# Performance work log

Measured on AMD Instinct MI355X. Metric: run time of the kernel, lower is better.

## Reference

```python
import jax, jax.numpy as jnp
import numpy as np

MAX_LENGTH = 11
SOS_TOKEN = 0
H = 256      # hidden_dim
V = 32000    # output_dim (vocab)
B = 256      # batch
S = 64       # encoder seq len


def setup_inputs() -> dict:
    key = jax.random.key(0)
    ks = jax.random.split(key, 16)
    sc = 0.05
    return {
        "encoder_outputs": jax.random.normal(ks[0], (B, S, H), jnp.float32),
        "encoder_hidden": jax.random.normal(ks[1], (1, B, H), jnp.float32),
        "target_tensor": jax.random.randint(ks[2], (B, MAX_LENGTH), 0, V),
        "embedding": jax.random.normal(ks[3], (V, H), jnp.float32) * sc,
        "Wa": jax.random.normal(ks[4], (H, H), jnp.float32) * sc,
        "ba": jnp.zeros((H,), jnp.float32),
        "Ua": jax.random.normal(ks[5], (H, H), jnp.float32) * sc,
        "bua": jnp.zeros((H,), jnp.float32),
        "Va": jax.random.normal(ks[6], (H, 1), jnp.float32) * sc,
        "bva": jnp.zeros((1,), jnp.float32),
        "W_ih": jax.random.normal(ks[7], (H, 2 * H), jnp.float32) * sc,
        "b_ih": jnp.zeros((H,), jnp.float32),
        "W_hh": jax.random.normal(ks[8], (H, H), jnp.float32) * sc,
        "b_hh": jnp.zeros((H,), jnp.float32),
        "W_out": jax.random.normal(ks[9], (V, H), jnp.float32) * sc,
        "b_out": jnp.zeros((V,), jnp.float32),
    }


def _decode(encoder_outputs, encoder_hidden, target_tensor,
            embedding, Wa, ba, Ua, bua, Va, bva,
            W_ih, b_ih, W_hh, b_hh, W_out, b_out):
    batch = encoder_outputs.shape[0]
    # Ua(keys) is step-invariant: precompute once.  [B, S, H]
    uk = jnp.einsum('bsh,kh->bsk', encoder_outputs, Ua) + bua
    h0 = encoder_hidden[0]  # [B, H]
    # teacher forcing: input at step i is SOS for i=0, else target[:, i-1]
    tokens = jnp.concatenate(
        [jnp.full((batch, 1), SOS_TOKEN, dtype=target_tensor.dtype),
         target_tensor[:, :MAX_LENGTH - 1]], axis=1)  # [B, T]

    def step(h, tok):
        emb = embedding[tok]                                   # [B, H]
        q = jnp.einsum('bh,kh->bk', h, Wa) + ba                # Wa(query)
        scores = jnp.tanh(q[:, None, :] + uk) @ Va + bva       # [B, S, 1]
        attn = jax.nn.softmax(scores[..., 0], axis=-1)         # [B, S]
        ctx = jnp.einsum('bs,bsh->bh', attn, encoder_outputs)  # [B, H]
        x = jnp.concatenate([emb, ctx], axis=-1)               # [B, 2H]
        h_new = jnp.tanh(x @ W_ih.T + b_ih + h @ W_hh.T + b_hh)
        logits = h_new @ W_out.T + b_out                       # [B, V]
        return h_new, (logits, attn)

    h_last, (logits, attns) = jax.lax.scan(step, h0, tokens.T)
    decoder_outputs = jax.nn.log_softmax(
        jnp.transpose(logits, (1, 0, 2)), axis=-1)             # [B, T, V]
    attentions = jnp.transpose(attns, (1, 0, 2))               # [B, T, S]
    return decoder_outputs, h_last[None], attentions


def reference(encoder_outputs, encoder_hidden, target_tensor,
              embedding, Wa, ba, Ua, bua, Va, bva,
              W_ih, b_ih, W_hh, b_hh, W_out, b_out):
    return _decode(encoder_outputs, encoder_hidden, target_tensor,
                   embedding, Wa, ba, Ua, bua, Va, bva,
                   W_ih, b_ih, W_hh, b_hh, W_out, b_out)
```

## Files before the change

kernel.cpp:

```cpp
#include <hip/hip_runtime.h>

#define Bz 256
#define Sz 64
#define Hz 256
#define Vz 32000
#define Tz 11
#define Mz (Bz*Tz)

typedef __attribute__((ext_vector_type(8))) short bf16x8;
typedef __attribute__((ext_vector_type(4))) float f32x4;

__device__ __forceinline__ float blo(unsigned int u){ return __builtin_bit_cast(float, u<<16); }
__device__ __forceinline__ float bhi(unsigned int u){ return __builtin_bit_cast(float, u & 0xffff0000u); }
__device__ __forceinline__ unsigned short f2bf(float f){
  unsigned int x = __builtin_bit_cast(unsigned int, f);
  return (unsigned short)((x + 0x7fffu + ((x>>16)&1u)) >> 16);
}
__device__ __forceinline__ float bf2f(unsigned short u){ return __builtin_bit_cast(float, ((unsigned int)u)<<16); }
__device__ __forceinline__ float ftanh(float x){ float e = __expf(2.f*x); return 1.f - 2.f/(e+1.f); }

__device__ __forceinline__ float dot8(uint4 wv, const float* base){
  float4 h0 = *(const float4*)(base);
  float4 h1 = *(const float4*)(base+4);
  return blo(wv.x)*h0.x + bhi(wv.x)*h0.y + blo(wv.y)*h0.z + bhi(wv.y)*h0.w
       + blo(wv.z)*h1.x + bhi(wv.z)*h1.y + blo(wv.w)*h1.z + bhi(wv.w)*h1.w;
}

__device__ __forceinline__ void gll16(const unsigned short* g, unsigned short* l){
  __builtin_amdgcn_global_load_lds(
      (const __attribute__((address_space(1))) unsigned int*)g,
      (__attribute__((address_space(3))) unsigned int*)l, 16, 0, 0);
}

__global__ __launch_bounds__(256) void k_prep(
    const float* __restrict__ Wa,
    const float* __restrict__ Wih, const float* __restrict__ Whh,
    const int* __restrict__ target, const float* __restrict__ embedding,
    const float* __restrict__ b_ih,
    const float* __restrict__ enc, const float* __restrict__ Ua,
    const float* __restrict__ bua,
    unsigned short* __restrict__ wa_p,
    unsigned short* __restrict__ wih2_p, unsigned short* __restrict__ whh_p,
    float* __restrict__ E, unsigned short* __restrict__ uk_b){
  __shared__ float rows[16][Hz];
  int tid = threadIdx.x;
  int bid = blockIdx.x;
  if (bid < 256){
    int i = bid*256 + tid;
    int k = i>>8, j = i&255;
    int p = ((j>>3)*256 + k)*8 + (j&7);
    wa_p[p]   = f2bf(Wa[i]);
    whh_p[p]  = f2bf(Whh[i]);
    wih2_p[p] = f2bf(Wih[k*512 + 256 + j]);
  } else if (bid < 256+176){
    int m0 = (bid-256)*16;
    for (int r=0;r<16;r++){
      int m = m0 + r; int b = m/11, t = m - b*11;
      int tok = (t==0) ? 0 : target[b*11 + (t-1)];
      rows[r][tid] = embedding[(size_t)tok*Hz + tid];
    }
    __syncthreads();
    float acc[16];
    #pragma unroll
    for (int r=0;r<16;r++) acc[r]=0.f;
    const float* wrow = Wih + tid*512;
    for (int j4=0;j4<64;j4++){
      float4 w = *(const float4*)(wrow + j4*4);
      #pragma unroll
      for (int r=0;r<16;r++){
        float4 e = *(const float4*)(&rows[r][j4*4]);
        acc[r] += w.x*e.x + w.y*e.y + w.z*e.z + w.w*e.w;
      }
    }
    float bi = b_ih[tid];
    for (int r=0;r<16;r++) E[(m0+r)*Hz + tid] = acc[r] + bi;
  } else {
    int r0 = (bid-(256+176))*16;
    for (int r=0;r<16;r++) rows[r][tid] = enc[(size_t)(r0+r)*Hz + tid];
    __syncthreads();
    float acc[16];
    #pragma unroll
    for (int r=0;r<16;r++) acc[r]=0.f;
    const float* wrow = Ua + tid*Hz;
    for (int j4=0;j4<64;j4++){
      float4 w = *(const float4*)(wrow + j4*4);
      #pragma unroll
      for (int r=0;r<16;r++){
        float4 e = *(const float4*)(&rows[r][j4*4]);
        acc[r] += w.x*e.x + w.y*e.y + w.z*e.z + w.w*e.w;
      }
    }
    float bk = bua[tid];
    for (int r=0;r<16;r++) uk_b[(size_t)(r0+r)*Hz + tid] = f2bf(acc[r] + bk);
  }
}

__global__ __launch_bounds__(512) __attribute__((amdgpu_waves_per_eu(2,4)))
void k_rnn(
    const float* __restrict__ enc, const float* __restrict__ ench,
    const float* __restrict__ ba, const float* __restrict__ Va,
    const float* __restrict__ bva, const float* __restrict__ b_hh,
    const unsigned short* __restrict__ uk_b, const unsigned short* __restrict__ wa_p,
    const unsigned short* __restrict__ wih2_p, const unsigned short* __restrict__ whh_p,
    const float* __restrict__ E, unsigned short* __restrict__ hs_b,
    float* __restrict__ out_hlast, float* __restrict__ out_attn,
    const float* __restrict__ Wout, unsigned short* __restrict__ wout_b){
  __shared__ __align__(16) unsigned short uk_lds[Sz][Hz];
  __shared__ __align__(16) unsigned short enc_lds[Sz][Hz];
  __shared__ __align__(16) float h_lds[Hz];
  __shared__ __align__(16) float q_lds[Hz];
  __shared__ __align__(16) float hh_lds[Hz];
  __shared__ __align__(16) float ctx_lds[Hz];
  __shared__ __align__(16) float redq[2][Hz];
  __shared__ __align__(16) float redh[2][Hz];
  __shared__ float sc_lds[Sz];
  __shared__ float attn_lds[Sz];
  int tid = threadIdx.x;

  if (blockIdx.x >= Bz){
    int i = (blockIdx.x - Bz)*512 + tid;
    const int stride = 1024*512;
    for (int idx = i; idx < Vz*Hz; idx += stride) wout_b[idx] = f2bf(Wout[idx]);
    return;
  }

  int b = blockIdx.x;
  int k = tid & 255, qd = tid >> 8;
  int lane = tid & 63, wv = tid >> 6;
  const int rot = (b & 3) << 2;

  {
    const uint4* src = (const uint4*)(uk_b + (size_t)b*Sz*Hz);
    uint4* dst = (uint4*)(&uk_lds[0][0]);
    #pragma unroll
    for (int i=0;i<4;i++) dst[i*512+tid] = src[i*512+tid];
  }
  {
    const float4* src = (const float4*)(enc + (size_t)b*Sz*Hz);
    #pragma unroll
    for (int i=0;i<8;i++){
      int idx = i*512 + tid;
      float4 v = src[idx];
      ushort4 p; p.x=f2bf(v.x); p.y=f2bf(v.y); p.z=f2bf(v.z); p.w=f2bf(v.w);
      *(ushort4*)((unsigned short*)(&enc_lds[0][0]) + idx*4) = p;
    }
  }
  if (tid < Hz) h_lds[tid] = ench[b*Hz + tid];
  float va_r[4];
  #pragma unroll
  for (int c=0;c<4;c++) va_r[c] = Va[lane + 64*c];
  float ba_k = ba[k], bhh_k = b_hh[k], bva_s = bva[0];

  const uint4* wap = (const uint4*)(wa_p)   + (size_t)qd*16*256 + k;
  const uint4* whp = (const uint4*)(whh_p)  + (size_t)qd*16*256 + k;
  const uint4* w2p = (const uint4*)(wih2_p) + (size_t)qd*16*256 + k;
  __syncthreads();

  for (int t=0; t<Tz; t++){
    int m = b*Tz + t;
    const float* hb = &h_lds[qd*128];
    {
      float a0=0.f, a1=0.f, a2=0.f, a3=0.f;
      #pragma unroll 2
      for (int jx=0;jx<16;jx+=4){
        int jj = (jx + rot) & 15;
        uint4 w0=wap[(jj+0)*256], w1=wap[(jj+1)*256], w2=wap[(jj+2)*256], w3=wap[(jj+3)*256];
        a0 += dot8(w0, hb + jj*8 +  0);
        a1 += dot8(w1, hb + jj*8 +  8);
        a2 += dot8(w2, hb + jj*8 + 16);
        a3 += dot8(w3, hb + jj*8 + 24);
      }
      redq[qd][k] = (a0+a1) + (a2+a3);
      float b0=0.f, b1=0.f, b2=0.f, b3=0.f;
      #pragma unroll 2
      for (int jx=0;jx<16;jx+=4){
        int jj = (jx + rot) & 15;
        uint4 w0=whp[(jj+0)*256], w1=whp[(jj+1)*256], w2=whp[(jj+2)*256], w3=whp[(jj+3)*256];
        b0 += dot8(w0, hb + jj*8 +  0);
        b1 += dot8(w1, hb + jj*8 +  8);
        b2 += dot8(w2, hb + jj*8 + 16);
        b3 += dot8(w3, hb + jj*8 + 24);
      }
      redh[qd][k] = (b0+b1) + (b2+b3);
    }
    __syncthreads();
    if (qd == 0) q_lds[k]  = redq[0][k] + redq[1][k] + ba_k;
    else         hh_lds[k] = redh[0][k] + redh[1][k];
    __syncthreads();
    {
      float ql[4];
      #pragma unroll
      for (int c=0;c<4;c++) ql[c] = q_lds[lane + 64*c];
      #pragma unroll
      for (int si=0; si<8; si++){
        int s = wv*8 + si;
        float p = 0.f;
        #pragma unroll
        for (int c=0;c<4;c++){
          float u = bf2f(uk_lds[s][lane + 64*c]);
          p += ftanh(ql[c] + u) * va_r[c];
        }
        #pragma unroll
        for (int off=1; off<64; off<<=1) p += __shfl_xor(p, off, 64);
        if (lane==0) sc_lds[s] = p + bva_s;
      }
    }
    __syncthreads();
    {
      float sv = sc_lds[lane];
      float mx = sv;
      #pragma unroll
      for (int off=1; off<64; off<<=1) mx = fmaxf(mx, __shfl_xor(mx, off, 64));
      float e = __expf(sv - mx);
      float sum = e;
      #pragma unroll
      for (int off=1; off<64; off<<=1) sum += __shfl_xor(sum, off, 64);
      float a = e / sum;
      if (wv == 0){
        attn_lds[lane] = a;
        out_attn[(size_t)m*Sz + lane] = a;
      }
    }
    __syncthreads();
    {
      float c0=0.f, c1=0.f;
      #pragma unroll
      for (int i=0;i<32;i+=2){
        int s = qd*32 + i;
        c0 += attn_lds[s]   * bf2f(enc_lds[s][k]);
        c1 += attn_lds[s+1] * bf2f(enc_lds[s+1][k]);
      }
      redq[qd][k] = c0 + c1;
    }
    __syncthreads();
    if (qd == 0) ctx_lds[k] = redq[0][k] + redq[1][k];
    __syncthreads();
    {
      const float* cb = &ctx_lds[qd*128];
      float a0=0.f, a1=0.f, a2=0.f, a3=0.f;
      #pragma unroll 2
      for (int jx=0;jx<16;jx+=4){
        int jj = (jx + rot) & 15;
        uint4 w0=w2p[(jj+0)*256], w1=w2p[(jj+1)*256], w2=w2p[(jj+2)*256], w3=w2p[(jj+3)*256];
        a0 += dot8(w0, cb + jj*8 +  0);
        a1 += dot8(w1, cb + jj*8 +  8);
        a2 += dot8(w2, cb + jj*8 + 16);
        a3 += dot8(w3, cb + jj*8 + 24);
      }
      redh[qd][k] = (a0+a1) + (a2+a3);
    }
    __syncthreads();
    if (qd == 0){
      float acc = E[(size_t)m*Hz+k] + bhh_k + hh_lds[k] + redh[0][k] + redh[1][k];
      float hn = ftanh(acc);
      h_lds[k] = hn;
      hs_b[(size_t)m*Hz + k] = f2bf(hn);
      if (t==Tz-1) out_hlast[b*Hz + k] = hn;
    }
    __syncthreads();
  }
}

__global__ __launch_bounds__(256) void k_gemm(
    const unsigned short* __restrict__ Ab, const unsigned short* __restrict__ Bb,
    const float* __restrict__ b_out, const float* __restrict__ lse,
    float* __restrict__ out, float* __restrict__ partials){
  __shared__ __align__(16) unsigned short As[128*64];
  __shared__ __align__(16) unsigned short Bs[128*64];
  int tid = threadIdx.x;
  int fid = blockIdx.x;
  int xcd = fid & 7, wu = fid >> 3;
  int wid = (xcd < 4 ? xcd*688 : 4*688 + (xcd-4)*687) + wu;
  int bn = wid / 22;
  int bm = wid - bn*22;
  int m0 = bm*128, n0 = bn*128;
  int w = tid>>6, lane = tid&63;
  int wm = w>>1, wn = w&1;
  f32x4 acc[4][4];
  #pragma unroll
  for (int i=0;i<4;i++)
    #pragma unroll
    for (int j=0;j<4;j++) acc[i][j] = (f32x4){0.f,0.f,0.f,0.f};

  for (int ktx=0; ktx<4; ktx++){
    int kt = (ktx + bm) & 3;
    __syncthreads();
    #pragma unroll
    for (int i=0;i<4;i++){
      int chunk = i*256 + tid;
      int row = chunk>>3, c8 = chunk&7;
      gll16(Ab + (size_t)(m0+row)*Hz + kt*64 + c8*8, &As[(i*256 + w*64)*8]);
      gll16(Bb + (size_t)(n0+row)*Hz + kt*64 + c8*8, &Bs[(i*256 + w*64)*8]);
    }
    __syncthreads();
    #pragma unroll
    for (int ks=0; ks<2; ks++){
      bf16x8 af[4], bg[4];
      #pragma unroll
      for (int i=0;i<4;i++){
        int row = wm*64 + i*16 + (lane&15);
        af[i] = *(const bf16x8*)(&As[row*64 + ks*32 + (lane>>4)*8]);
      }
      #pragma unroll
      for (int j=0;j<4;j++){
        int row = wn*64 + j*16 + (lane&15);
        bg[j] = *(const bf16x8*)(&Bs[row*64 + ks*32 + (lane>>4)*8]);
      }
      #pragma unroll
      for (int i=0;i<4;i++)
        #pragma unroll
        for (int j=0;j<4;j++)
          acc[i][j] = __builtin_amdgcn_mfma_f32_16x16x32_bf16(af[i], bg[j], acc[i][j], 0,0,0);
    }
  }
  int col_l = lane & 15, rgrp = lane >> 4;
  if (lse == nullptr){
    #pragma unroll
    for (int i=0;i<4;i++){
      int rowbase = m0 + wm*64 + i*16 + rgrp*4;
      #pragma unroll
      for (int r=0;r<4;r++){
        float se = 0.f;
        #pragma unroll
        for (int j=0;j<4;j++){
          int col = n0 + wn*64 + j*16 + col_l;
          se += __expf(acc[i][j][r] + b_out[col]);
        }
        se += __shfl_xor(se,1,64); se += __shfl_xor(se,2,64);
        se += __shfl_xor(se,4,64); se += __shfl_xor(se,8,64);
        if (col_l == 0) partials[(size_t)(bn*2+wn)*Mz + rowbase + r] = se;
      }
    }
  } else {
    #pragma unroll
    for (int i=0;i<4;i++){
      int rowbase = m0 + wm*64 + i*16 + rgrp*4;
      #pragma unroll
      for (int r=0;r<4;r++){
        float l = lse[rowbase + r];
        #pragma unroll
        for (int j=0;j<4;j++){
          int col = n0 + wn*64 + j*16 + col_l;
          out[(size_t)(rowbase+r)*Vz + col] = acc[i][j][r] + b_out[col] - l;
        }
      }
    }
  }
}

__global__ __launch_bounds__(256) void k_lse(const float* __restrict__ partials,
                                             float* __restrict__ lse){
  int m = blockIdx.x*256 + threadIdx.x;
  if (m < Mz){
    float s = 0.f;
    for (int c=0;c<500;c++) s += partials[(size_t)c*Mz + m];
    lse[m] = logf(s);
  }
}

extern "C" void kernel_launch(void* const* d_in, const int* in_sizes, int n_in,
                              void* d_out, int out_size, void* d_ws, size_t ws_size,
                              hipStream_t stream) {
  const float* enc   = (const float*)d_in[0];
  const float* ench  = (const float*)d_in[1];
  const int*   target= (const int*)d_in[2];
  const float* emb   = (const float*)d_in[3];
  const float* Wa    = (const float*)d_in[4];
  const float* ba    = (const float*)d_in[5];
  const float* Ua    = (const float*)d_in[6];
  const float* bua   = (const float*)d_in[7];
  const float* Va    = (const float*)d_in[8];
  const float* bva   = (const float*)d_in[9];
  const float* Wih   = (const float*)d_in[10];
  const float* bih   = (const float*)d_in[11];
  const float* Whh   = (const float*)d_in[12];
  const float* bhh   = (const float*)d_in[13];
  const float* Wout  = (const float*)d_in[14];
  const float* bout  = (const float*)d_in[15];

  float* out = (float*)d_out;
  float* out_logits = out;
  float* out_hlast  = out + (size_t)Mz*Vz;
  float* out_attn   = out_hlast + Bz*Hz;

  char* ws = (char*)d_ws;
  unsigned short* wout_b = (unsigned short*)(ws);
  unsigned short* wa_p   = (unsigned short*)(ws + 16384000);
  unsigned short* wih2_p = (unsigned short*)(ws + 16515072);
  unsigned short* whh_p  = (unsigned short*)(ws + 16646144);
  unsigned short* hs_b   = (unsigned short*)(ws + 16777216);
  float*          lse    = (float*)(ws + 18219008);

  char* sc = (char*)d_out;
  unsigned short* uk_b     = (unsigned short*)(sc);
  float*          E        = (float*)(sc + 8388608);
  float*          partials = (float*)(sc + 11272192);

  k_prep <<<256+176+1024, 256, 0, stream>>>(Wa, Wih, Whh,
                                            target, emb, bih, enc, Ua, bua,
                                            wa_p, wih2_p, whh_p, E, uk_b);
  k_rnn  <<<Bz+1024, 512, 0, stream>>>(enc, ench, ba, Va, bva, bhh,
                                       uk_b, wa_p, wih2_p, whh_p, E, hs_b,
                                       out_hlast, out_attn, Wout, wout_b);
  k_gemm <<<5500, 256, 0, stream>>>(hs_b, wout_b, bout, nullptr, out_logits, partials);
  k_lse  <<<11, 256, 0, stream>>>(partials, lse);
  k_gemm <<<5500, 256, 0, stream>>>(hs_b, wout_b, bout, lse, out_logits, partials);
}
```

Baseline: 400.8 us.

## Precompute W_ih context projection of encoder outputs to drop per-step matvec

Uses linearity: W_ih_ctx·(attn·enc) = attn·(W_ih_ctx·enc), so the prep kernel now projects every encoder output row through the context half of W_ih once and stores it in bf16. The recurrent kernel loads this projected tensor into LDS in place of the raw encoder outputs. The attention-weighted sum then yields the context term directly, removing a 256x256 matvec and two barriers from every serial step. The cost is extra parallel prep work (a B*S x H x H GEMM) and an extra bf16 scratch buffer. Precision shifts slightly because the projection is rounded to bf16 before the weighted sum.

```diff
diff --git a/kernel.cpp b/kernel.cpp
--- a/kernel.cpp
+++ b/kernel.cpp
@@ -39,9 +39,9 @@
     const float* __restrict__ b_ih,
     const float* __restrict__ enc, const float* __restrict__ Ua,
     const float* __restrict__ bua,
-    unsigned short* __restrict__ wa_p,
-    unsigned short* __restrict__ wih2_p, unsigned short* __restrict__ whh_p,
-    float* __restrict__ E, unsigned short* __restrict__ uk_b){
+    unsigned short* __restrict__ wa_p, unsigned short* __restrict__ whh_p,
+    float* __restrict__ E, unsigned short* __restrict__ uk_b,
+    unsigned short* __restrict__ w2e_b){
   __shared__ float rows[16][Hz];
   int tid = threadIdx.x;
   int bid = blockIdx.x;
@@ -51,7 +51,6 @@
     int p = ((j>>3)*256 + k)*8 + (j&7);
     wa_p[p]   = f2bf(Wa[i]);
     whh_p[p]  = f2bf(Whh[i]);
-    wih2_p[p] = f2bf(Wih[k*512 + 256 + j]);
   } else if (bid < 256+176){
     int m0 = (bid-256)*16;
     for (int r=0;r<16;r++){
@@ -74,7 +73,7 @@
     }
     float bi = b_ih[tid];
     for (int r=0;r<16;r++) E[(m0+r)*Hz + tid] = acc[r] + bi;
-  } else {
+  } else if (bid < 256+176+1024){
     int r0 = (bid-(256+176))*16;
     for (int r=0;r<16;r++) rows[r][tid] = enc[(size_t)(r0+r)*Hz + tid];
     __syncthreads();
@@ -92,25 +91,41 @@
     }
     float bk = bua[tid];
     for (int r=0;r<16;r++) uk_b[(size_t)(r0+r)*Hz + tid] = f2bf(acc[r] + bk);
+  } else {
+    int r0 = (bid-(256+176+1024))*16;
+    for (int r=0;r<16;r++) rows[r][tid] = enc[(size_t)(r0+r)*Hz + tid];
+    __syncthreads();
+    float acc[16];
+    #pragma unroll
+    for (int r=0;r<16;r++) acc[r]=0.f;
+    const float* wrow = Wih + tid*512 + 256;
+    for (int j4=0;j4<64;j4++){
+      float4 w = *(const float4*)(wrow + j4*4);
+      #pragma unroll
+      for (int r=0;r<16;r++){
+        float4 e = *(const float4*)(&rows[r][j4*4]);
+        acc[r] += w.x*e.x + w.y*e.y + w.z*e.z + w.w*e.w;
+      }
+    }
+    for (int r=0;r<16;r++) w2e_b[(size_t)(r0+r)*Hz + tid] = f2bf(acc[r]);
   }
 }
 
 __global__ __launch_bounds__(512) __attribute__((amdgpu_waves_per_eu(2,4)))
 void k_rnn(
-    const float* __restrict__ enc, const float* __restrict__ ench,
+    const float* __restrict__ ench,
     const float* __restrict__ ba, const float* __restrict__ Va,
     const float* __restrict__ bva, const float* __restrict__ b_hh,
     const unsigned short* __restrict__ uk_b, const unsigned short* __restrict__ wa_p,
-    const unsigned short* __restrict__ wih2_p, const unsigned short* __restrict__ whh_p,
+    const unsigned short* __restrict__ whh_p, const unsigned short* __restrict__ w2e_b,
     const float* __restrict__ E, unsigned short* __restrict__ hs_b,
     float* __restrict__ out_hlast, float* __restrict__ out_attn,
     const float* __restrict__ Wout, unsigned short* __restrict__ wout_b){
   __shared__ __align__(16) unsigned short uk_lds[Sz][Hz];
-  __shared__ __align__(16) unsigned short enc_lds[Sz][Hz];
+  __shared__ __align__(16) unsigned short w2e_lds[Sz][Hz];
   __shared__ __align__(16) float h_lds[Hz];
   __shared__ __align__(16) float q_lds[Hz];
   __shared__ __align__(16) float hh_lds[Hz];
-  __shared__ __align__(16) float ctx_lds[Hz];
   __shared__ __align__(16) float redq[2][Hz];
   __shared__ __align__(16) float redh[2][Hz];
   __shared__ float sc_lds[Sz];
@@ -130,19 +145,14 @@
   const int rot = (b & 3) << 2;
 
   {
-    const uint4* src = (const uint4*)(uk_b + (size_t)b*Sz*Hz);
-    uint4* dst = (uint4*)(&uk_lds[0][0]);
-    #pragma unroll
-    for (int i=0;i<4;i++) dst[i*512+tid] = src[i*512+tid];
-  }
-  {
-    const float4* src = (const float4*)(enc + (size_t)b*Sz*Hz);
-    #pragma unroll
-    for (int i=0;i<8;i++){
-      int idx = i*512 + tid;
-      float4 v = src[idx];
-      ushort4 p; p.x=f2bf(v.x); p.y=f2bf(v.y); p.z=f2bf(v.z); p.w=f2bf(v.w);
-      *(ushort4*)((unsigned short*)(&enc_lds[0][0]) + idx*4) = p;
+    const uint4* src1 = (const uint4*)(uk_b  + (size_t)b*Sz*Hz);
+    const uint4* src2 = (const uint4*)(w2e_b + (size_t)b*Sz*Hz);
+    uint4* dst1 = (uint4*)(&uk_lds[0][0]);
+    uint4* dst2 = (uint4*)(&w2e_lds[0][0]);
+    #pragma unroll
+    for (int i=0;i<4;i++){
+      dst1[i*512+tid] = src1[i*512+tid];
+      dst2[i*512+tid] = src2[i*512+tid];
     }
   }
   if (tid < Hz) h_lds[tid] = ench[b*Hz + tid];
@@ -151,9 +161,8 @@
   for (int c=0;c<4;c++) va_r[c] = Va[lane + 64*c];
   float ba_k = ba[k], bhh_k = b_hh[k], bva_s = bva[0];
 
-  const uint4* wap = (const uint4*)(wa_p)   + (size_t)qd*16*256 + k;
-  const uint4* whp = (const uint4*)(whh_p)  + (size_t)qd*16*256 + k;
-  const uint4* w2p = (const uint4*)(wih2_p) + (size_t)qd*16*256 + k;
+  const uint4* wap = (const uint4*)(wa_p)  + (size_t)qd*16*256 + k;
+  const uint4* whp = (const uint4*)(whh_p) + (size_t)qd*16*256 + k;
   __syncthreads();
 
   for (int t=0; t<Tz; t++){
@@ -227,31 +236,14 @@
       #pragma unroll
       for (int i=0;i<32;i+=2){
         int s = qd*32 + i;
-        c0 += attn_lds[s]   * bf2f(enc_lds[s][k]);
-        c1 += attn_lds[s+1] * bf2f(enc_lds[s+1][k]);
+        c0 += attn_lds[s]   * bf2f(w2e_lds[s][k]);
+        c1 += attn_lds[s+1] * bf2f(w2e_lds[s+1][k]);
       }
       redq[qd][k] = c0 + c1;
     }
     __syncthreads();
-    if (qd == 0) ctx_lds[k] = redq[0][k] + redq[1][k];
-    __syncthreads();
-    {
-      const float* cb = &ctx_lds[qd*128];
-      float a0=0.f, a1=0.f, a2=0.f, a3=0.f;
-      #pragma unroll 2
-      for (int jx=0;jx<16;jx+=4){
-        int jj = (jx + rot) & 15;
-        uint4 w0=w2p[(jj+0)*256], w1=w2p[(jj+1)*256], w2=w2p[(jj+2)*256], w3=w2p[(jj+3)*256];
-        a0 += dot8(w0, cb + jj*8 +  0);
-        a1 += dot8(w1, cb + jj*8 +  8);
-        a2 += dot8(w2, cb + jj*8 + 16);
-        a3 += dot8(w3, cb + jj*8 + 24);
-      }
-      redh[qd][k] = (a0+a1) + (a2+a3);
-    }
-    __syncthreads();
     if (qd == 0){
-      float acc = E[(size_t)m*Hz+k] + bhh_k + hh_lds[k] + redh[0][k] + redh[1][k];
+      float acc = E[(size_t)m*Hz+k] + bhh_k + hh_lds[k] + redq[0][k] + redq[1][k];
       float hn = ftanh(acc);
       h_lds[k] = hn;
       hs_b[(size_t)m*Hz + k] = f2bf(hn);
@@ -386,8 +378,7 @@
   char* ws = (char*)d_ws;
   unsigned short* wout_b = (unsigned short*)(ws);
   unsigned short* wa_p   = (unsigned short*)(ws + 16384000);
-  unsigned short* wih2_p = (unsigned short*)(ws + 16515072);
-  unsigned short* whh_p  = (unsigned short*)(ws + 16646144);
+  unsigned short* whh_p  = (unsigned short*)(ws + 16515072);
   unsigned short* hs_b   = (unsigned short*)(ws + 16777216);
   float*          lse    = (float*)(ws + 18219008);
 
@@ -395,12 +386,13 @@
   unsigned short* uk_b     = (unsigned short*)(sc);
   float*          E        = (float*)(sc + 8388608);
   float*          partials = (float*)(sc + 11272192);
-
-  k_prep <<<256+176+1024, 256, 0, stream>>>(Wa, Wih, Whh,
+  unsigned short* w2e_b    = (unsigned short*)(sc + 16904192);
+
+  k_prep <<<256+176+1024+1024, 256, 0, stream>>>(Wa, Wih, Whh,
                                             target, emb, bih, enc, Ua, bua,
-                                            wa_p, wih2_p, whh_p, E, uk_b);
-  k_rnn  <<<Bz+1024, 512, 0, stream>>>(enc, ench, ba, Va, bva, bhh,
-                                       uk_b, wa_p, wih2_p, whh_p, E, hs_b,
+                                            wa_p, whh_p, E, uk_b, w2e_b);
+  k_rnn  <<<Bz+1024, 512, 0, stream>>>(ench, ba, Va, bva, bhh,
+                                       uk_b, wa_p, whh_p, w2e_b, E, hs_b,
                                        out_hlast, out_attn, Wout, wout_b);
   k_gemm <<<5500, 256, 0, stream>>>(hs_b, wout_b, bout, nullptr, out_logits, partials);
   k_lse  <<<11, 256, 0, stream>>>(partials, lse);
```

Result: slower. 467.9 us (+16.7%).
